# Optimization experiments

Hardware: AMD Instinct MI355X
Metric: run time of the kernel (lower is better)

The kernel has to match this reference:

```python
import jax, jax.numpy as jnp
import numpy as np

D = 1024   # cfg.hid (downscaled from 8192)
M = 20000  # cfg.mem_c // 2 (downscaled)
B, LQ = 4, 8
PLAST_S = 0.05
IMPORTANCE = 1.0


def mha_shared_kv(q, kv_k, kv_v, Wi, bi, Wo, bo, nheads):
    """torch nn.MultiheadAttention (batch_first) with batch-shared K/V.
    q: [B,Lq,D]; kv_k/kv_v: [Lk,D] shared across batch (avoids the .repeat()
    materialization in the original torch code while computing identical math)."""
    dh = D // nheads
    Wq, Wk, Wv = jnp.split(Wi, 3, axis=0)
    bq, bk, bv = jnp.split(bi, 3)
    qp = (jnp.einsum('bqd,ed->bqe', q, Wq) + bq) * (dh ** -0.5)
    kp = kv_k @ Wk.T + bk              # [Lk,D]
    vp = kv_v @ Wv.T + bv              # [Lk,D]
    qh = qp.reshape(q.shape[0], q.shape[1], nheads, dh)      # [B,Lq,h,dh]
    kh = kp.reshape(kp.shape[0], nheads, dh)                 # [Lk,h,dh]
    vh = vp.reshape(vp.shape[0], nheads, dh)                 # [Lk,h,dh]
    scores = jnp.einsum('bqhd,khd->bhqk', qh, kh)            # [B,h,Lq,Lk]
    attn = jax.nn.softmax(scores, axis=-1)
    ctx = jnp.einsum('bhqk,khd->bqhd', attn, vh)
    ctx = ctx.reshape(q.shape[0], q.shape[1], D)
    return ctx @ Wo.T + bo


def setup_inputs() -> dict:
    key = jax.random.key(0)
    ks = jax.random.split(key, 16)
    s = 0.02
    return {
        'q':    jax.random.normal(ks[0], (B, LQ, D), jnp.float32),
        'data': jax.random.normal(ks[1], (B, D), jnp.float32),
        'ek':   jax.random.normal(ks[2], (M, D), jnp.float32),
        'ev':   jax.random.normal(ks[3], (M, D), jnp.float32),
        'sk':   jax.random.normal(ks[4], (M, D), jnp.float32),
        'sv':   jax.random.normal(ks[5], (M, D), jnp.float32),
        'wm':   jax.random.normal(ks[6], (10, D), jnp.float32),
        'Wi_e': jax.random.normal(ks[7], (3 * D, D), jnp.float32) * s,
        'bi_e': jnp.zeros((3 * D,), jnp.float32),
        'Wo_e': jax.random.normal(ks[8], (D, D), jnp.float32) * s,
        'bo_e': jnp.zeros((D,), jnp.float32),
        'Wi_s': jax.random.normal(ks[9], (3 * D, D), jnp.float32) * s,
        'bi_s': jnp.zeros((3 * D,), jnp.float32),
        'Wo_s': jax.random.normal(ks[10], (D, D), jnp.float32) * s,
        'bo_s': jnp.zeros((D,), jnp.float32),
        'Wi_w': jax.random.normal(ks[11], (3 * D, D), jnp.float32) * s,
        'bi_w': jnp.zeros((3 * D,), jnp.float32),
        'Wo_w': jax.random.normal(ks[12], (D, D), jnp.float32) * s,
        'bo_w': jnp.zeros((D,), jnp.float32),
        'Wrp':  jax.random.normal(ks[13], (D, 3 * D), jnp.float32) * s,
        'brp':  jnp.zeros((D,), jnp.float32),
        'eu':   jnp.zeros((M,), jnp.float32),
    }


def reference(q, data, ek, ev, sk, sv, wm,
              Wi_e, bi_e, Wo_e, bo_e,
              Wi_s, bi_s, Wo_s, bo_s,
              Wi_w, bi_w, Wo_w, bo_w,
              Wrp, brp, eu):
    # ---- NeuroMemory.read ----
    e_r = mha_shared_kv(q, ek, ev, Wi_e, bi_e, Wo_e, bo_e, 16)
    s_r = mha_shared_kv(q, sk, sv, Wi_s, bi_s, Wo_s, bo_s, 16)
    w_r = mha_shared_kv(q, wm, wm, Wi_w, bi_w, Wo_w, bo_w, 8)
    read_out = jnp.concatenate([e_r, s_r, w_r], axis=-1) @ Wrp.T + brp  # [B,Lq,D]

    # ---- NeuroMemory.write (episodic, Hebbian plasticity update) ----
    scores = data @ ek.T                       # [B,M]
    probs = jax.nn.softmax(scores, axis=-1)    # [B,M]
    upd = probs * (PLAST_S * IMPORTANCE)       # [B,M]
    u = upd.mean(axis=0)[:, None]              # [M,1] (batch-mean update strength)
    d = data.mean(axis=0)[None, :]             # [1,D]
    new_ek = ek * (1.0 - u) + d * u            # [M,D]
    new_ev = ev * (1.0 - u) + d * u            # [M,D]
    new_eu = eu * 0.99 + jax.lax.stop_gradient(probs.sum(axis=0))  # [M]
    return (read_out, new_ek, new_ev, new_eu)
```

## Files before the change

### kernel.cpp

```cpp
#include <hip/hip_runtime.h>
#include <hip/hip_fp16.h>
#include <hip/hip_bf16.h>
#include <cstdint>
#include <cstddef>

#define D_HID 1024
#define MEM_M 20000
#define NBATCH 4
#define BL 32
#define NROWS 512
#define SROWS_E 516
#define SROWS_S 512
#define BK 32
#define LDT 40
#define PV_NC 16

typedef __attribute__((ext_vector_type(8))) short short8;
typedef __attribute__((ext_vector_type(4))) float f32x4;
typedef __attribute__((ext_vector_type(16))) float f32x16;
typedef __attribute__((ext_vector_type(4))) unsigned short us4;

__device__ inline ushort f2bf(float f) {
    __hip_bfloat16 b = __float2bfloat16(f);
    return *reinterpret_cast<ushort*>(&b);
}
__device__ inline float h2f(ushort u) {
    __half h; *reinterpret_cast<ushort*>(&h) = u; return __half2float(h);
}

__device__ __forceinline__ void block_sync_lds() {
    asm volatile("s_waitcnt lgkmcnt(0)" ::: "memory");
    __builtin_amdgcn_s_barrier();
}

struct SkDesc  { const float* A; const float* B; int K; int M; };
struct SkDescs { SkDesc d[5]; };
struct RdDesc  { const float* bias; float* dst; int M; int ldc; float alpha; };
struct RdDescs { RdDesc d[5]; };

__device__ __forceinline__ void skinny_body(const SkDesc dd, float* __restrict__ part,
                                            int gk, int k0, int n0, int tid)
{
    __shared__ float As[32][132];
    __shared__ float Bs[64][129];
    const int K = dd.K, M = dd.M;
    {
        const int r = tid >> 3, cbl = (tid & 7) * 16;
        if (r < M) {
            const float* src = dd.A + (size_t)r * K + k0 + cbl;
            #pragma unroll
            for (int i = 0; i < 4; ++i) {
                const float4 v = *(const float4*)(src + i * 4);
                As[r][cbl + i * 4 + 0] = v.x; As[r][cbl + i * 4 + 1] = v.y;
                As[r][cbl + i * 4 + 2] = v.z; As[r][cbl + i * 4 + 3] = v.w;
            }
        } else {
            #pragma unroll
            for (int i = 0; i < 16; ++i) As[r][cbl + i] = 0.f;
        }
    }
    {
        const int r = tid >> 2, cbl = (tid & 3) * 32;
        const float* src = dd.B + (size_t)(n0 + r) * K + k0 + cbl;
        #pragma unroll
        for (int i = 0; i < 8; ++i) {
            const float4 v = *(const float4*)(src + i * 4);
            Bs[r][cbl + i * 4 + 0] = v.x; Bs[r][cbl + i * 4 + 1] = v.y;
            Bs[r][cbl + i * 4 + 2] = v.z; Bs[r][cbl + i * 4 + 3] = v.w;
        }
    }
    __syncthreads();
    const int n = tid & 63, mg = tid >> 6;
    float acc[8];
    #pragma unroll
    for (int i = 0; i < 8; ++i) acc[i] = 0.f;
    #pragma unroll 4
    for (int k = 0; k < 128; k += 4) {
        const float b0 = Bs[n][k + 0], b1 = Bs[n][k + 1];
        const float b2 = Bs[n][k + 2], b3 = Bs[n][k + 3];
        #pragma unroll
        for (int i = 0; i < 8; ++i) {
            const float4 a = *(const float4*)&As[mg * 8 + i][k];
            acc[i] = fmaf(a.x, b0, fmaf(a.y, b1, fmaf(a.z, b2, fmaf(a.w, b3, acc[i]))));
        }
    }
    #pragma unroll
    for (int i = 0; i < 8; ++i)
        part[((size_t)gk * 32 + mg * 8 + i) * 1024 + n0 + n] = acc[i];
}

__global__ __launch_bounds__(256)
void k_skinny(SkDescs ds, float* __restrict__ part)
{
    skinny_body(ds.d[blockIdx.z], part,
                blockIdx.z * gridDim.y + blockIdx.y,
                blockIdx.y * 128, blockIdx.x * 64, threadIdx.x);
}

__global__ __launch_bounds__(256)
void k_head(SkDescs ds, float* __restrict__ part,
            const float* __restrict__ ek, const float* __restrict__ sk,
            ushort* __restrict__ kvb)
{
    const int bx = blockIdx.x;
    const int tid = threadIdx.x;
    if (bx < 640) {
        const int g = bx >> 7;
        const int rem = bx & 127;
        const int kc = rem >> 4;
        const int n0 = (rem & 15) * 64;
        skinny_body(ds.d[g], part, g * 8 + kc, kc * 128, n0, tid);
    } else {
        const size_t nchunks = (size_t)2 * MEM_M * D_HID / 8;
        for (size_t i = (size_t)(bx - 640) * 256 + tid; i < nchunks;
             i += (size_t)1408 * 256) {
            const size_t base = i * 8;
            const float* src = (base < (size_t)MEM_M * D_HID)
                             ? (ek + base) : (sk + base - (size_t)MEM_M * D_HID);
            const float4 v0 = *(const float4*)(src);
            const float4 v1 = *(const float4*)(src + 4);
            alignas(16) ushort o[8];
            o[0] = f2bf(v0.x); o[1] = f2bf(v0.y); o[2] = f2bf(v0.z); o[3] = f2bf(v0.w);
            o[4] = f2bf(v1.x); o[5] = f2bf(v1.y); o[6] = f2bf(v1.z); o[7] = f2bf(v1.w);
            *(short8*)(kvb + base) = *(const short8*)o;
        }
    }
}

__global__ __launch_bounds__(256)
void k_skred(RdDescs ds, const float* __restrict__ part, int nkc)
{
    const int g = blockIdx.y;
    const int m = blockIdx.x;
    const RdDesc dd = ds.d[g];
    if (m >= dd.M) return;
    const int c = threadIdx.x * 4;
    float4 s = make_float4(0.f, 0.f, 0.f, 0.f);
    for (int kc = 0; kc < nkc; ++kc) {
        const float4 v = *(const float4*)&part[((size_t)(g * nkc + kc) * 32 + m) * 1024 + c];
        s.x += v.x; s.y += v.y; s.z += v.z; s.w += v.w;
    }
    const float4 b = *(const float4*)(dd.bias + c);
    float4 o;
    o.x = (s.x + b.x) * dd.alpha; o.y = (s.y + b.y) * dd.alpha;
    o.z = (s.z + b.z) * dd.alpha; o.w = (s.w + b.w) * dd.alpha;
    *(float4*)(dd.dst + (size_t)m * dd.ldc + c) = o;
}

__global__ __launch_bounds__(256)
void mfma_scores(const ushort* __restrict__ A_e, const ushort* __restrict__ ekb,
                 const ushort* __restrict__ A_s, const ushort* __restrict__ skb,
                 __half* __restrict__ S_e, __half* __restrict__ S_s,
                 const float* __restrict__ c0_e, const float* __restrict__ c0_s)
{
    __shared__ ushort As[2][128][LDT];
    __shared__ ushort Bs[2][128][LDT];
    const int tid = threadIdx.x;
    const int i = blockIdx.x + 9 * blockIdx.y;
    const int xcd = i & 7, idx = i >> 3;
    const int wg = (xcd < 5 ? xcd * 177 : 885 + (xcd - 5) * 176) + idx;
    const int mi = wg % 9, nbk = wg / 9;
    const int bank = (mi >= 5);
    const int m0 = (bank ? (mi - 5) : mi) * 128;
    const int n0 = nbk * 128;
    const ushort* __restrict__ A = bank ? A_s : A_e;
    const ushort* __restrict__ B = bank ? skb : ekb;
    __half* __restrict__ S = bank ? S_s : S_e;
    const float* __restrict__ c0 = bank ? c0_s : c0_e;
    const int Mreal = bank ? SROWS_S : SROWS_E;

    const int wid = tid >> 6, lane = tid & 63;
    const int wr = (wid >> 1) * 64, wc = (wid & 1) * 64;
    const int l31 = lane & 31, l2 = lane >> 5;

    const int srow = tid >> 1;
    const int ac = (tid & 1) * 16;
    int gbrow = n0 + srow; if (gbrow > MEM_M - 1) gbrow = MEM_M - 1;
    const ushort* Ap = A + (size_t)(m0 + srow) * 1024 + ac;
    const ushort* Bp = B + (size_t)gbrow * 1024 + ac;

    f32x16 acc[2][2];
    #pragma unroll
    for (int fm = 0; fm < 2; ++fm)
        #pragma unroll
        for (int fn = 0; fn < 2; ++fn)
            #pragma unroll
            for (int r = 0; r < 16; ++r) acc[fm][fn][r] = 0.f;

    auto MF = [&](int bu) {
        short8 a[2][2], b[2][2];
        #pragma unroll
        for (int f = 0; f < 2; ++f)
            #pragma unroll
            for (int kh = 0; kh < 2; ++kh) {
                a[f][kh] = *(const short8*)&As[bu][wr + f * 32 + l31][kh * 16 + l2 * 8];
                b[f][kh] = *(const short8*)&Bs[bu][wc + f * 32 + l31][kh * 16 + l2 * 8];
            }
        #pragma unroll
        for (int fm = 0; fm < 2; ++fm)
            #pragma unroll
            for (int fn = 0; fn < 2; ++fn)
                #pragma unroll
                for (int kh = 0; kh < 2; ++kh)
                    acc[fm][fn] = __builtin_amdgcn_mfma_f32_32x32x16_bf16(
                        a[fm][kh], b[fn][kh], acc[fm][fn], 0, 0, 0);
    };

    short8 a00, a01, b00, b01;
    short8 a10, a11, b10, b11;

#define SC_LOAD0(KT) { a00 = *(const short8*)(Ap + (KT)); a01 = *(const short8*)(Ap + (KT) + 8); \
                       b00 = *(const short8*)(Bp + (KT)); b01 = *(const short8*)(Bp + (KT) + 8); }
#define SC_LOAD1(KT) { a10 = *(const short8*)(Ap + (KT)); a11 = *(const short8*)(Ap + (KT) + 8); \
                       b10 = *(const short8*)(Bp + (KT)); b11 = *(const short8*)(Bp + (KT) + 8); }
#define SC_STORE0(BU) { *(short8*)&As[BU][srow][ac] = a00; *(short8*)&As[BU][srow][ac + 8] = a01; \
                        *(short8*)&Bs[BU][srow][ac] = b00; *(short8*)&Bs[BU][srow][ac + 8] = b01; }
#define SC_STORE1(BU) { *(short8*)&As[BU][srow][ac] = a10; *(short8*)&As[BU][srow][ac + 8] = a11; \
                        *(short8*)&Bs[BU][srow][ac] = b10; *(short8*)&Bs[BU][srow][ac + 8] = b11; }

    SC_LOAD0(0);
    SC_LOAD1(32);
    SC_STORE0(0);
    block_sync_lds();
    for (int it = 0; it < 16; ++it) {
        const int kt = it * 64;
        if (it < 15) SC_LOAD0(kt + 64);
        MF(0);
        SC_STORE1(1);
        block_sync_lds();
        if (it < 15) SC_LOAD1(kt + 96);
        MF(1);
        if (it < 15) SC_STORE0(0);
        block_sync_lds();
    }
#undef SC_LOAD0
#undef SC_LOAD1
#undef SC_STORE0
#undef SC_STORE1

    #pragma unroll
    for (int fm = 0; fm < 2; ++fm) {
        #pragma unroll
        for (int fn = 0; fn < 2; ++fn) {
            #pragma unroll
            for (int r = 0; r < 16; ++r) {
                const int row = m0 + wr + fm * 32 + (r & 3) + 8 * (r >> 2) + 4 * l2;
                if (row >= Mreal) continue;
                const int col = n0 + wc + fn * 32 + l31;
                if (col < MEM_M)
                    S[(size_t)row * MEM_M + col] = __float2half(acc[fm][fn][r] + c0[row]);
            }
        }
    }
}

__global__ __launch_bounds__(256)
void mfma_pv(const ushort* __restrict__ P_e, const ushort* __restrict__ P_s,
             const float* __restrict__ ev, const float* __restrict__ sv,
             float* __restrict__ part)
{
    __shared__ ushort As[2][128][LDT];
    __shared__ ushort Bs[2][128][LDT];
    const int tid = threadIdx.x;
    const int z = blockIdx.z;
    const int bank = z >> 4, c = z & 15;
    const ushort* __restrict__ P = bank ? P_s : P_e;
    const float* __restrict__ V = bank ? sv : ev;
    const int m0 = blockIdx.y * 128, n0 = blockIdx.x * 128;
    const int ks0 = (c * 625) / PV_NC, ks1 = ((c + 1) * 625) / PV_NC;
    const int wid = tid >> 6, lane = tid & 63;
    const int wr = (wid >> 1) * 64, wc = (wid & 1) * 64;
    const int l31 = lane & 31, l2 = lane >> 5;
    const int kb = (tid & 7) * 4, nb2 = (tid >> 3) * 4;
    const int srow = tid >> 1, ac = (tid & 1) * 16;
    const ushort* Pp = P + (size_t)(m0 + srow) * MEM_M + ac;

    f32x16 acc[2][2];
    #pragma unroll
    for (int fm = 0; fm < 2; ++fm)
        #pragma unroll
        for (int fn = 0; fn < 2; ++fn)
            #pragma unroll
            for (int r = 0; r < 16; ++r) acc[fm][fn][r] = 0.f;

    auto MF = [&](int bu) {
        short8 a[2][2], b[2][2];
        #pragma unroll
        for (int f = 0; f < 2; ++f)
            #pragma unroll
            for (int kh = 0; kh < 2; ++kh) {
                a[f][kh] = *(const short8*)&As[bu][wr + f * 32 + l31][kh * 16 + l2 * 8];
                b[f][kh] = *(const short8*)&Bs[bu][wc + f * 32 + l31][kh * 16 + l2 * 8];
            }
        #pragma unroll
        for (int fm = 0; fm < 2; ++fm)
            #pragma unroll
            for (int fn = 0; fn < 2; ++fn)
                #pragma unroll
                for (int kh = 0; kh < 2; ++kh)
                    acc[fm][fn] = __builtin_amdgcn_mfma_f32_32x32x16_bf16(
                        a[fm][kh], b[fn][kh], acc[fm][fn], 0, 0, 0);
    };

    short8 pa00, pa01, pa10, pa11;
    float4 q00, q01, q02, q03, q10, q11, q12, q13;

#define PV_LOAD0(T) { const int kt = (T) * 32; \
    pa00 = *(const short8*)(Pp + kt); pa01 = *(const short8*)(Pp + kt + 8); \
    q00 = *(const float4*)(V + (size_t)(kt + kb + 0) * 1024 + n0 + nb2); \
    q01 = *(const float4*)(V + (size_t)(kt + kb + 1) * 1024 + n0 + nb2); \
    q02 = *(const float4*)(V + (size_t)(kt + kb + 2) * 1024 + n0 + nb2); \
    q03 = *(const float4*)(V + (size_t)(kt + kb + 3) * 1024 + n0 + nb2); }
#define PV_LOAD1(T) { const int kt = (T) * 32; \
    pa10 = *(const short8*)(Pp + kt); pa11 = *(const short8*)(Pp + kt + 8); \
    q10 = *(const float4*)(V + (size_t)(kt + kb + 0) * 1024 + n0 + nb2); \
    q11 = *(const float4*)(V + (size_t)(kt + kb + 1) * 1024 + n0 + nb2); \
    q12 = *(const float4*)(V + (size_t)(kt + kb + 2) * 1024 + n0 + nb2); \
    q13 = *(const float4*)(V + (size_t)(kt + kb + 3) * 1024 + n0 + nb2); }
#define PV_STORE0(BU) { \
    *(short8*)&As[BU][srow][ac] = pa00; *(short8*)&As[BU][srow][ac + 8] = pa01; \
    us4 w; \
    w.x = f2bf(q00.x); w.y = f2bf(q01.x); w.z = f2bf(q02.x); w.w = f2bf(q03.x); \
    *(us4*)&Bs[BU][nb2 + 0][kb] = w; \
    w.x = f2bf(q00.y); w.y = f2bf(q01.y); w.z = f2bf(q02.y); w.w = f2bf(q03.y); \
    *(us4*)&Bs[BU][nb2 + 1][kb] = w; \
    w.x = f2bf(q00.z); w.y = f2bf(q01.z); w.z = f2bf(q02.z); w.w = f2bf(q03.z); \
    *(us4*)&Bs[BU][nb2 + 2][kb] = w; \
    w.x = f2bf(q00.w); w.y = f2bf(q01.w); w.z = f2bf(q02.w); w.w = f2bf(q03.w); \
    *(us4*)&Bs[BU][nb2 + 3][kb] = w; }
#define PV_STORE1(BU) { \
    *(short8*)&As[BU][srow][ac] = pa10; *(short8*)&As[BU][srow][ac + 8] = pa11; \
    us4 w; \
    w.x = f2bf(q10.x); w.y = f2bf(q11.x); w.z = f2bf(q12.x); w.w = f2bf(q13.x); \
    *(us4*)&Bs[BU][nb2 + 0][kb] = w; \
    w.x = f2bf(q10.y); w.y = f2bf(q11.y); w.z = f2bf(q12.y); w.w = f2bf(q13.y); \
    *(us4*)&Bs[BU][nb2 + 1][kb] = w; \
    w.x = f2bf(q10.z); w.y = f2bf(q11.z); w.z = f2bf(q12.z); w.w = f2bf(q13.z); \
    *(us4*)&Bs[BU][nb2 + 2][kb] = w; \
    w.x = f2bf(q10.w); w.y = f2bf(q11.w); w.z = f2bf(q12.w); w.w = f2bf(q13.w); \
    *(us4*)&Bs[BU][nb2 + 3][kb] = w; }

    PV_LOAD0(ks0);
    if (ks0 + 1 < ks1) PV_LOAD1(ks0 + 1);
    PV_STORE0(0);
    block_sync_lds();
    for (int t = ks0; t < ks1; t += 2) {
        if (t + 2 < ks1) PV_LOAD0(t + 2);
        MF(0);
        if (t + 1 < ks1) PV_STORE1(1);
        block_sync_lds();
        if (t + 1 < ks1) {
            if (t + 3 < ks1) PV_LOAD1(t + 3);
            MF(1);
            if (t + 2 < ks1) PV_STORE0(0);
            block_sync_lds();
        }
    }
#undef PV_LOAD0
#undef PV_LOAD1
#undef PV_STORE0
#undef PV_STORE1

    float* __restrict__ po = part + (size_t)z * NROWS * 1024;
    #pragma unroll
    for (int fm = 0; fm < 2; ++fm)
        #pragma unroll
        for (int fn = 0; fn < 2; ++fn)
            #pragma unroll
            for (int r = 0; r < 16; ++r) {
                const int row = m0 + wr + fm * 32 + (r & 3) + 8 * (r >> 2) + 4 * l2;
                const int col = n0 + wc + fn * 32 + l31;
                po[(size_t)row * 1024 + col] = acc[fm][fn][r];
            }
}

__global__ __launch_bounds__(256)
void k_T(const float* __restrict__ qp,
         const float* __restrict__ Wi_e, const float* __restrict__ bi_e,
         const float* __restrict__ Wi_s, const float* __restrict__ bi_s,
         ushort* __restrict__ A_e, float* __restrict__ c0_e,
         ushort* __restrict__ A_s, float* __restrict__ c0_s,
         const float* __restrict__ data, float* __restrict__ dmean)
{
    const int bq = blockIdx.x;
    const int tid = threadIdx.x;
    if (bq >= 128) {
        if (bq < 252) {
            const int row = SROWS_E + (bq - 128);
            us4 z4; z4.x = 0; z4.y = 0; z4.z = 0; z4.w = 0;
            *(us4*)(A_e + (size_t)row * 1024 + tid * 4) = z4;
        } else {
            for (int t = tid; t < D_HID; t += 256) {
                float s = 0.f;
                #pragma unroll
                for (int b = 0; b < NBATCH; ++b) s += data[b * D_HID + t];
                dmean[t] = 0.25f * s;
                #pragma unroll
                for (int b = 0; b < NBATCH; ++b)
                    A_e[(size_t)(NROWS + b) * 1024 + t] = f2bf(data[b * D_HID + t]);
            }
            if (tid < NBATCH) c0_e[NROWS + tid] = 0.f;
        }
        return;
    }
    const int bank = bq >> 6;
    const int h = (bq >> 2) & 15;
    const int q4 = bq & 3;
    const float* qpB = qp + (size_t)bank * BL * D_HID;
    const float* Wk = (bank ? Wi_s : Wi_e) + (size_t)D_HID * D_HID;
    const float* bk = (bank ? bi_s : bi_e) + D_HID;
    ushort* T  = bank ? A_s : A_e;
    float* c0 = bank ? c0_s : c0_e;

    __shared__ float qs[32][64];
    for (int i = tid; i < 32 * 64; i += 256) {
        const int r = i >> 6, j = i & 63;
        qs[r][j] = qpB[(size_t)r * D_HID + h * 64 + j];
    }
    __syncthreads();
    const int e = q4 * 256 + tid;
    float acc[32];
    #pragma unroll
    for (int r = 0; r < 32; ++r) acc[r] = 0.f;
    for (int j = 0; j < 64; ++j) {
        const float w = Wk[(size_t)(h * 64 + j) * D_HID + e];
        #pragma unroll
        for (int r = 0; r < 32; ++r) acc[r] = fmaf(qs[r][j], w, acc[r]);
    }
    #pragma unroll
    for (int r = 0; r < 32; ++r) T[(size_t)(r * 16 + h) * 1024 + e] = f2bf(acc[r]);
    if (q4 == 0 && tid < 32) {
        float s = 0.f;
        for (int j = 0; j < 64; ++j) s += qs[tid][j] * bk[h * 64 + j];
        c0[tid * 16 + h] = s;
    }
}

__global__ __launch_bounds__(256)
void k_softmax(__half* __restrict__ S_e, __half* __restrict__ S_s,
               float* __restrict__ mrow, float* __restrict__ lrow)
{
    const int row = blockIdx.x;
    ushort* p = (row < SROWS_E) ? (ushort*)(S_e + (size_t)row * MEM_M)
                                : (ushort*)(S_s + (size_t)(row - SROWS_E) * MEM_M);
    const bool conv = (row < SROWS_E) ? (row < NROWS) : true;
    __shared__ float red_m[256];
    __shared__ float red_l[256];
    const int tid = threadIdx.x;
    float m = -3.0e38f, l = 0.f;
    for (int c = tid; c < MEM_M / 8; c += 256) {
        alignas(16) ushort t[8];
        *(short8*)t = *(const short8*)(p + c * 8);
        float v[8];
        #pragma unroll
        for (int j = 0; j < 8; ++j) v[j] = h2f(t[j]);
        float cm = v[0];
        #pragma unroll
        for (int j = 1; j < 8; ++j) cm = fmaxf(cm, v[j]);
        const float nm = fmaxf(m, cm);
        float s = 0.f;
        #pragma unroll
        for (int j = 0; j < 8; ++j) s += __expf(v[j] - nm);
        l = l * __expf(m - nm) + s;
        m = nm;
    }
    red_m[tid] = m; red_l[tid] = l; __syncthreads();
    for (int s = 128; s > 0; s >>= 1) {
        if (tid < s) {
            const float m2 = fmaxf(red_m[tid], red_m[tid + s]);
            red_l[tid] = red_l[tid] * __expf(red_m[tid] - m2)
                       + red_l[tid + s] * __expf(red_m[tid + s] - m2);
            red_m[tid] = m2;
        }
        __syncthreads();
    }
    const float rm = red_m[0];
    if (conv) {
        for (int c = tid; c < MEM_M / 8; c += 256) {
            alignas(16) ushort t[8];
            *(short8*)t = *(const short8*)(p + c * 8);
            alignas(16) ushort o[8];
            #pragma unroll
            for (int j = 0; j < 8; ++j) o[j] = f2bf(__expf(h2f(t[j]) - rm));
            *(short8*)(p + c * 8) = *(const short8*)o;
        }
    }
    if (tid == 0) { mrow[row] = rm; lrow[row] = red_l[0]; }
}

__global__ __launch_bounds__(256)
void k_uk(const __half* __restrict__ S_e,
          const float* __restrict__ mrow, const float* __restrict__ lrow,
          const float* __restrict__ eu,
          float* __restrict__ u, float* __restrict__ out_eu)
{
    const int k = blockIdx.x * 256 + threadIdx.x;
    if (k >= MEM_M) return;
    float sp = 0.f;
    #pragma unroll
    for (int b = 0; b < NBATCH; ++b) {
        const int row = NROWS + b;
        sp += __expf(__half2float(S_e[(size_t)row * MEM_M + k]) - mrow[row]) / lrow[row];
    }
    u[k] = 0.05f * 0.25f * sp;
    out_eu[k] = eu[k] * 0.99f + sp;
}

__global__ __launch_bounds__(256)
void k_pvred_upd(const float* __restrict__ part, const float* __restrict__ lrow,
                 float* __restrict__ R,
                 const float* __restrict__ ev, const float* __restrict__ u,
                 const float* __restrict__ dmean, float* __restrict__ out_ev)
{
    const int tid = threadIdx.x;
    if (blockIdx.x < 1024) {
        const size_t perb4 = (size_t)NROWS * 1024 / 4;
        const size_t i = (size_t)blockIdx.x * 256 + tid;
        const int bank = i >= perb4;
        const size_t off4 = i - (size_t)bank * perb4;
        const int m = (int)(off4 >> 8);
        const float inv = 1.f / lrow[bank ? (SROWS_E + m) : m];
        const float4* p = (const float4*)part + (size_t)bank * PV_NC * perb4 + off4;
        float4 s = make_float4(0.f, 0.f, 0.f, 0.f);
        #pragma unroll
        for (int c = 0; c < PV_NC; ++c) {
            const float4 v = p[(size_t)c * perb4];
            s.x += v.x; s.y += v.y; s.z += v.z; s.w += v.w;
        }
        s.x *= inv; s.y *= inv; s.z *= inv; s.w *= inv;
        ((float4*)R)[i] = s;
    } else {
        const int bid = blockIdx.x - 1024;
        const size_t n4 = (size_t)MEM_M * D_HID / 4;
        for (size_t i = (size_t)bid * 256 + tid; i < n4; i += (size_t)1024 * 256) {
            const int k = (int)(i >> 8);
            const int c = (int)(i & 255);
            const float uk = u[k];
            const float om = 1.f - uk;
            const float4 dd = ((const float4*)dmean)[c];
            const float4 b = ((const float4*)ev)[i];
            float4 ob;
            ob.x = b.x * om + dd.x * uk; ob.y = b.y * om + dd.y * uk;
            ob.z = b.z * om + dd.z * uk; ob.w = b.w * om + dd.w * uk;
            ((float4*)out_ev)[i] = ob;
        }
    }
}

__global__ __launch_bounds__(256)
void k_tail(const float* __restrict__ R,
            const float* __restrict__ Wi_e, const float* __restrict__ bi_e,
            const float* __restrict__ Wi_s, const float* __restrict__ bi_s,
            float* __restrict__ ctx,
            const float* __restrict__ qp, const float* __restrict__ kpw,
            const float* __restrict__ vpw,
            const float* __restrict__ ek, const float* __restrict__ u,
            const float* __restrict__ dmean, float* __restrict__ out_ek)
{
    __shared__ float sm[12384];
    const int tid = threadIdx.x;
    const int bx = blockIdx.x;
    if (bx < 32) {
        const int bank = bx >> 4;
        const int h = bx & 15;
        const float* Rb = R + (size_t)bank * NROWS * D_HID;
        const float* Wv = (bank ? Wi_s : Wi_e) + (size_t)2 * D_HID * D_HID;
        const float* bv = (bank ? bi_s : bi_e) + 2 * D_HID;
        float* cb = ctx + (size_t)bank * BL * D_HID;
        float (*Rs)[129] = (float(*)[129])sm;
        float (*Ws)[129] = (float(*)[129])(sm + 32 * 129);
        const int j = tid & 63;
        const int g = tid >> 6;
        float acc[8];
        #pragma unroll
        for (int i = 0; i < 8; ++i) acc[i] = 0.f;
        for (int ec = 0; ec < D_HID; ec += 128) {
            for (int i = tid; i < 32 * 128; i += 256) {
                const int r = i >> 7, e = i & 127;
                Rs[r][e] = Rb[(size_t)(r * 16 + h) * D_HID + ec + e];
            }
            for (int i = tid; i < 64 * 128; i += 256) {
                const int r = i >> 7, e = i & 127;
                Ws[r][e] = Wv[(size_t)(h * 64 + r) * D_HID + ec + e];
            }
            __syncthreads();
            for (int e = 0; e < 128; ++e) {
                const float w = Ws[j][e];
                #pragma unroll
                for (int i = 0; i < 8; ++i)
                    acc[i] = fmaf(Rs[g + 4 * i][e], w, acc[i]);
            }
            __syncthreads();
        }
        #pragma unroll
        for (int i = 0; i < 8; ++i) {
            const int bl = g + 4 * i;
            cb[(size_t)bl * D_HID + h * 64 + j] = acc[i] + bv[h * 64 + j];
        }
    } else if (bx < 64) {
        const int bl = bx - 32;
        float* q = sm;
        float (*kp)[1024] = (float(*)[1024])(sm + 1024);
        float (*pp)[10] = (float(*)[10])(sm + 1024 + 10240);
        const float* qrow = qp + (size_t)(2 * BL + bl) * D_HID;
        for (int i = tid; i < D_HID; i += 256) q[i] = qrow[i];
        for (int i = tid; i < 10 * D_HID; i += 256) kp[i >> 10][i & 1023] = kpw[i];
        __syncthreads();
        if (tid < 80) {
            const int h = tid / 10, k = tid % 10;
            float s = 0.f;
            for (int jj = 0; jj < 128; ++jj) s += q[h * 128 + jj] * kp[k][h * 128 + jj];
            pp[h][k] = s;
        }
        __syncthreads();
        if (tid < 8) {
            float m = -3.0e38f;
            for (int k = 0; k < 10; ++k) m = fmaxf(m, pp[tid][k]);
            float e[10]; float l = 0.f;
            for (int k = 0; k < 10; ++k) { e[k] = __expf(pp[tid][k] - m); l += e[k]; }
            const float inv = 1.f / l;
            for (int k = 0; k < 10; ++k) pp[tid][k] = e[k] * inv;
        }
        __syncthreads();
        float* cw = ctx + (size_t)(2 * BL + bl) * D_HID;
        for (int f = tid; f < D_HID; f += 256) {
            const int h = f >> 7;
            float s = 0.f;
            #pragma unroll
            for (int k = 0; k < 10; ++k) s += pp[h][k] * vpw[(size_t)k * D_HID + f];
            cw[f] = s;
        }
    } else {
        const int bid = bx - 64;
        const size_t n4 = (size_t)MEM_M * D_HID / 4;
        for (size_t i = (size_t)bid * 256 + tid; i < n4; i += (size_t)1024 * 256) {
            const int k = (int)(i >> 8);
            const int c = (int)(i & 255);
            const float uk = u[k];
            const float om = 1.f - uk;
            const float4 dd = ((const float4*)dmean)[c];
            const float4 a = ((const float4*)ek)[i];
            float4 oa;
            oa.x = a.x * om + dd.x * uk; oa.y = a.y * om + dd.y * uk;
            oa.z = a.z * om + dd.z * uk; oa.w = a.w * om + dd.w * uk;
            ((float4*)out_ek)[i] = oa;
        }
    }
}

extern "C" void kernel_launch(void* const* d_in, const int* in_sizes, int n_in,
                              void* d_out, int out_size, void* d_ws, size_t ws_size,
                              hipStream_t stream)
{
    (void)in_sizes; (void)n_in; (void)out_size; (void)ws_size;
    const float* q    = (const float*)d_in[0];
    const float* data = (const float*)d_in[1];
    const float* ek   = (const float*)d_in[2];
    const float* ev   = (const float*)d_in[3];
    const float* sk   = (const float*)d_in[4];
    const float* sv   = (const float*)d_in[5];
    const float* wm   = (const float*)d_in[6];
    const float* Wi_e = (const float*)d_in[7];
    const float* bi_e = (const float*)d_in[8];
    const float* Wo_e = (const float*)d_in[9];
    const float* bo_e = (const float*)d_in[10];
    const float* Wi_s = (const float*)d_in[11];
    const float* bi_s = (const float*)d_in[12];
    const float* Wo_s = (const float*)d_in[13];
    const float* bo_s = (const float*)d_in[14];
    const float* Wi_w = (const float*)d_in[15];
    const float* bi_w = (const float*)d_in[16];
    const float* Wo_w = (const float*)d_in[17];
    const float* bo_w = (const float*)d_in[18];
    const float* Wrp  = (const float*)d_in[19];
    const float* brp  = (const float*)d_in[20];
    const float* eu   = (const float*)d_in[21];

    float* out = (float*)d_out;
    float* out_read = out;
    float* out_ek = out + 32768;
    float* out_ev = out_ek + 20480000;
    float* out_eu = out_ev + 20480000;

    float* ws    = (float*)d_ws;
    float* qp    = ws;
    float* A_e   = qp + 98304;
    float* A_s   = A_e + 655360;
    float* c0_e  = A_s + 524288;
    float* c0_s  = c0_e + 640;
    float* dmean = c0_s + 512;
    float* u     = dmean + 1024;
    float* mrow  = u + 20480;
    float* lrow  = mrow + 1032;
    float* kpw   = lrow + 1032;
    float* vpw   = kpw + 10240;
    float* ctx   = vpw + 10240;
    float* cat   = ctx + 98304;
    float* skpart = cat + 98304;
    float* Rbuf  = skpart;

    ushort* A_e16 = (ushort*)A_e;
    ushort* A_s16 = (ushort*)A_s;

    ushort* ekb = (ushort*)out_ek;
    ushort* skb = ekb + (size_t)MEM_M * D_HID;
    float* part = out_ek;
    __half* S_e = (__half*)out_ev;
    __half* S_s = S_e + (size_t)SROWS_E * MEM_M;

    const dim3 b256(256);
    const float sc16 = 0.125f;
    const float sc8  = 0.08838834764831845f;

    SkDescs s1;
    s1.d[0] = {q,  Wi_e,            1024, 32};
    s1.d[1] = {q,  Wi_s,            1024, 32};
    s1.d[2] = {q,  Wi_w,            1024, 32};
    s1.d[3] = {wm, Wi_w + 1048576,  1024, 10};
    s1.d[4] = {wm, Wi_w + 2097152,  1024, 10};
    k_head<<<2048, b256, 0, stream>>>(s1, skpart, ek, sk, ekb);
    RdDescs r1;
    r1.d[0] = {bi_e,        qp,         32, 1024, sc16};
    r1.d[1] = {bi_s,        qp + 32768, 32, 1024, sc16};
    r1.d[2] = {bi_w,        qp + 65536, 32, 1024, sc8};
    r1.d[3] = {bi_w + 1024, kpw,        10, 1024, 1.f};
    r1.d[4] = {bi_w + 2048, vpw,        10, 1024, 1.f};
    k_skred<<<dim3(32, 5), b256, 0, stream>>>(r1, skpart, 8);

    k_T<<<253, b256, 0, stream>>>(qp, Wi_e, bi_e, Wi_s, bi_s,
                                  A_e16, c0_e, A_s16, c0_s, data, dmean);

    mfma_scores<<<dim3(9, 157), b256, 0, stream>>>(A_e16, ekb, A_s16, skb,
                                                   S_e, S_s, c0_e, c0_s);

    k_softmax<<<SROWS_E + SROWS_S, b256, 0, stream>>>(S_e, S_s, mrow, lrow);
    k_uk<<<79, b256, 0, stream>>>(S_e, mrow, lrow, eu, u, out_eu);

    mfma_pv<<<dim3(8, 4, 2 * PV_NC), b256, 0, stream>>>(
        (const ushort*)S_e, (const ushort*)S_s, ev, sv, part);

    k_pvred_upd<<<2048, b256, 0, stream>>>(part, lrow, Rbuf, ev, u, dmean, out_ev);

    k_tail<<<1088, b256, 0, stream>>>(Rbuf, Wi_e, bi_e, Wi_s, bi_s, ctx,
                                      qp, kpw, vpw, ek, u, dmean, out_ek);

    SkDescs s2;
    s2.d[0] = {ctx,         Wo_e, 1024, 32};
    s2.d[1] = {ctx + 32768, Wo_s, 1024, 32};
    s2.d[2] = {ctx + 65536, Wo_w, 1024, 32};
    s2.d[3] = {ctx,         Wo_e, 1024, 32};
    s2.d[4] = {ctx,         Wo_e, 1024, 32};
    k_skinny<<<dim3(16, 8, 3), b256, 0, stream>>>(s2, skpart);
    RdDescs r2;
    r2.d[0] = {bo_e, cat,        32, 3072, 1.f};
    r2.d[1] = {bo_s, cat + 1024, 32, 3072, 1.f};
    r2.d[2] = {bo_w, cat + 2048, 32, 3072, 1.f};
    r2.d[3] = r2.d[0];
    r2.d[4] = r2.d[0];
    k_skred<<<dim3(32, 3), b256, 0, stream>>>(r2, skpart, 8);

    SkDescs s3;
    s3.d[0] = {cat, Wrp, 3072, 32};
    s3.d[1] = s3.d[0]; s3.d[2] = s3.d[0]; s3.d[3] = s3.d[0]; s3.d[4] = s3.d[0];
    k_skinny<<<dim3(16, 24, 1), b256, 0, stream>>>(s3, skpart);
    RdDescs r3;
    r3.d[0] = {brp, out_read, 32, 1024, 1.f};
    r3.d[1] = r3.d[0]; r3.d[2] = r3.d[0]; r3.d[3] = r3.d[0]; r3.d[4] = r3.d[0];
    k_skred<<<dim3(32, 1), b256, 0, stream>>>(r3, skpart, 24);
}
```

Before: 487.6 us.

## Pre-convert value banks to bf16 during softmax and remap PV workgroups

Extra blocks in the softmax launch convert ev and sv from fp32 to bf16 buffers, so the PV GEMM reads half the bytes and skips per-tile conversion. The PV kernel now uses fewer K-splits (8 instead of 16) and an XCD-aware swizzle of workgroup ids. The write-scores rows move to a separate scratch buffer so the output buffers can be repacked to hold the bf16 copies and partials. The cost is an extra pass of roughly 160 MB of fp32 reads and 80 MB of bf16 writes, and the PV grid is halved, which may reduce parallelism.

```diff
diff --git a/kernel.cpp b/kernel.cpp
--- a/kernel.cpp
+++ b/kernel.cpp
@@ -13,7 +13,7 @@
 #define SROWS_S 512
 #define BK 32
 #define LDT 40
-#define PV_NC 16
+#define PV_NC 8
 
 typedef __attribute__((ext_vector_type(8))) short short8;
 typedef __attribute__((ext_vector_type(4))) float f32x4;
@@ -151,6 +151,7 @@
 void mfma_scores(const ushort* __restrict__ A_e, const ushort* __restrict__ ekb,
                  const ushort* __restrict__ A_s, const ushort* __restrict__ skb,
                  __half* __restrict__ S_e, __half* __restrict__ S_s,
+                 __half* __restrict__ swr,
                  const float* __restrict__ c0_e, const float* __restrict__ c0_s)
 {
     __shared__ ushort As[2][128][LDT];
@@ -165,7 +166,6 @@
     const int n0 = nbk * 128;
     const ushort* __restrict__ A = bank ? A_s : A_e;
     const ushort* __restrict__ B = bank ? skb : ekb;
-    __half* __restrict__ S = bank ? S_s : S_e;
     const float* __restrict__ c0 = bank ? c0_s : c0_e;
     const int Mreal = bank ? SROWS_S : SROWS_E;
 
@@ -247,8 +247,11 @@
                 const int row = m0 + wr + fm * 32 + (r & 3) + 8 * (r >> 2) + 4 * l2;
                 if (row >= Mreal) continue;
                 const int col = n0 + wc + fn * 32 + l31;
-                if (col < MEM_M)
-                    S[(size_t)row * MEM_M + col] = __float2half(acc[fm][fn][r] + c0[row]);
+                if (col >= MEM_M) continue;
+                const __half hv = __float2half(acc[fm][fn][r] + c0[row]);
+                if (bank) S_s[(size_t)row * MEM_M + col] = hv;
+                else if (row < NROWS) S_e[(size_t)row * MEM_M + col] = hv;
+                else swr[(size_t)(row - NROWS) * MEM_M + col] = hv;
             }
         }
     }
@@ -256,17 +259,20 @@
 
 __global__ __launch_bounds__(256)
 void mfma_pv(const ushort* __restrict__ P_e, const ushort* __restrict__ P_s,
-             const float* __restrict__ ev, const float* __restrict__ sv,
+             const ushort* __restrict__ evb, const ushort* __restrict__ svb,
              float* __restrict__ part)
 {
     __shared__ ushort As[2][128][LDT];
     __shared__ ushort Bs[2][128][LDT];
     const int tid = threadIdx.x;
-    const int z = blockIdx.z;
-    const int bank = z >> 4, c = z & 15;
+    const int bid = blockIdx.x + 8 * (blockIdx.y + 4 * blockIdx.z);
+    const int wgs = (bid & 7) * 64 + (bid >> 3);
+    const int nI = wgs & 7, mI = (wgs >> 3) & 3;
+    const int z = wgs >> 5;
+    const int bank = z >> 3, c = z & 7;
     const ushort* __restrict__ P = bank ? P_s : P_e;
-    const float* __restrict__ V = bank ? sv : ev;
-    const int m0 = blockIdx.y * 128, n0 = blockIdx.x * 128;
+    const ushort* __restrict__ Vb = bank ? svb : evb;
+    const int m0 = mI * 128, n0 = nI * 128;
     const int ks0 = (c * 625) / PV_NC, ks1 = ((c + 1) * 625) / PV_NC;
     const int wid = tid >> 6, lane = tid & 63;
     const int wr = (wid >> 1) * 64, wc = (wid & 1) * 64;
@@ -303,41 +309,41 @@
     };
 
     short8 pa00, pa01, pa10, pa11;
-    float4 q00, q01, q02, q03, q10, q11, q12, q13;
+    us4 q0[4], q1[4];
 
 #define PV_LOAD0(T) { const int kt = (T) * 32; \
     pa00 = *(const short8*)(Pp + kt); pa01 = *(const short8*)(Pp + kt + 8); \
-    q00 = *(const float4*)(V + (size_t)(kt + kb + 0) * 1024 + n0 + nb2); \
-    q01 = *(const float4*)(V + (size_t)(kt + kb + 1) * 1024 + n0 + nb2); \
-    q02 = *(const float4*)(V + (size_t)(kt + kb + 2) * 1024 + n0 + nb2); \
-    q03 = *(const float4*)(V + (size_t)(kt + kb + 3) * 1024 + n0 + nb2); }
+    q0[0] = *(const us4*)(Vb + (size_t)(kt + kb + 0) * 1024 + n0 + nb2); \
+    q0[1] = *(const us4*)(Vb + (size_t)(kt + kb + 1) * 1024 + n0 + nb2); \
+    q0[2] = *(const us4*)(Vb + (size_t)(kt + kb + 2) * 1024 + n0 + nb2); \
+    q0[3] = *(const us4*)(Vb + (size_t)(kt + kb + 3) * 1024 + n0 + nb2); }
 #define PV_LOAD1(T) { const int kt = (T) * 32; \
     pa10 = *(const short8*)(Pp + kt); pa11 = *(const short8*)(Pp + kt + 8); \
-    q10 = *(const float4*)(V + (size_t)(kt + kb + 0) * 1024 + n0 + nb2); \
-    q11 = *(const float4*)(V + (size_t)(kt + kb + 1) * 1024 + n0 + nb2); \
-    q12 = *(const float4*)(V + (size_t)(kt + kb + 2) * 1024 + n0 + nb2); \
-    q13 = *(const float4*)(V + (size_t)(kt + kb + 3) * 1024 + n0 + nb2); }
+    q1[0] = *(const us4*)(Vb + (size_t)(kt + kb + 0) * 1024 + n0 + nb2); \
+    q1[1] = *(const us4*)(Vb + (size_t)(kt + kb + 1) * 1024 + n0 + nb2); \
+    q1[2] = *(const us4*)(Vb + (size_t)(kt + kb + 2) * 1024 + n0 + nb2); \
+    q1[3] = *(const us4*)(Vb + (size_t)(kt + kb + 3) * 1024 + n0 + nb2); }
 #define PV_STORE0(BU) { \
     *(short8*)&As[BU][srow][ac] = pa00; *(short8*)&As[BU][srow][ac + 8] = pa01; \
     us4 w; \
-    w.x = f2bf(q00.x); w.y = f2bf(q01.x); w.z = f2bf(q02.x); w.w = f2bf(q03.x); \
+    w.x = q0[0].x; w.y = q0[1].x; w.z = q0[2].x; w.w = q0[3].x; \
     *(us4*)&Bs[BU][nb2 + 0][kb] = w; \
-    w.x = f2bf(q00.y); w.y = f2bf(q01.y); w.z = f2bf(q02.y); w.w = f2bf(q03.y); \
+    w.x = q0[0].y; w.y = q0[1].y; w.z = q0[2].y; w.w = q0[3].y; \
     *(us4*)&Bs[BU][nb2 + 1][kb] = w; \
-    w.x = f2bf(q00.z); w.y = f2bf(q01.z); w.z = f2bf(q02.z); w.w = f2bf(q03.z); \
+    w.x = q0[0].z; w.y = q0[1].z; w.z = q0[2].z; w.w = q0[3].z; \
     *(us4*)&Bs[BU][nb2 + 2][kb] = w; \
-    w.x = f2bf(q00.w); w.y = f2bf(q01.w); w.z = f2bf(q02.w); w.w = f2bf(q03.w); \
+    w.x = q0[0].w; w.y = q0[1].w; w.z = q0[2].w; w.w = q0[3].w; \
     *(us4*)&Bs[BU][nb2 + 3][kb] = w; }
 #define PV_STORE1(BU) { \
     *(short8*)&As[BU][srow][ac] = pa10; *(short8*)&As[BU][srow][ac + 8] = pa11; \
     us4 w; \
-    w.x = f2bf(q10.x); w.y = f2bf(q11.x); w.z = f2bf(q12.x); w.w = f2bf(q13.x); \
+    w.x = q1[0].x; w.y = q1[1].x; w.z = q1[2].x; w.w = q1[3].x; \
     *(us4*)&Bs[BU][nb2 + 0][kb] = w; \
-    w.x = f2bf(q10.y); w.y = f2bf(q11.y); w.z = f2bf(q12.y); w.w = f2bf(q13.y); \
+    w.x = q1[0].y; w.y = q1[1].y; w.z = q1[2].y; w.w = q1[3].y; \
     *(us4*)&Bs[BU][nb2 + 1][kb] = w; \
-    w.x = f2bf(q10.z); w.y = f2bf(q11.z); w.z = f2bf(q12.z); w.w = f2bf(q13.z); \
+    w.x = q1[0].z; w.y = q1[1].z; w.z = q1[2].z; w.w = q1[3].z; \
     *(us4*)&Bs[BU][nb2 + 2][kb] = w; \
-    w.x = f2bf(q10.w); w.y = f2bf(q11.w); w.z = f2bf(q12.w); w.w = f2bf(q13.w); \
+    w.x = q1[0].w; w.y = q1[1].w; w.z = q1[2].w; w.w = q1[3].w; \
     *(us4*)&Bs[BU][nb2 + 3][kb] = w; }
 
     PV_LOAD0(ks0);
@@ -438,15 +444,37 @@
 
 __global__ __launch_bounds__(256)
 void k_softmax(__half* __restrict__ S_e, __half* __restrict__ S_s,
-               float* __restrict__ mrow, float* __restrict__ lrow)
-{
-    const int row = blockIdx.x;
-    ushort* p = (row < SROWS_E) ? (ushort*)(S_e + (size_t)row * MEM_M)
-                                : (ushort*)(S_s + (size_t)(row - SROWS_E) * MEM_M);
-    const bool conv = (row < SROWS_E) ? (row < NROWS) : true;
+               __half* __restrict__ swr,
+               float* __restrict__ mrow, float* __restrict__ lrow,
+               const float* __restrict__ ev, const float* __restrict__ sv,
+               ushort* __restrict__ evb, ushort* __restrict__ svb)
+{
+    const int bx = blockIdx.x;
+    const int tid = threadIdx.x;
+    if (bx >= SROWS_E + SROWS_S) {
+        const size_t nchunks = (size_t)2 * MEM_M * D_HID / 8;
+        for (size_t i = (size_t)(bx - (SROWS_E + SROWS_S)) * 256 + tid; i < nchunks;
+             i += (size_t)1408 * 256) {
+            const size_t base = i * 8;
+            const bool second = base >= (size_t)MEM_M * D_HID;
+            const float* src = second ? (sv + base - (size_t)MEM_M * D_HID) : (ev + base);
+            ushort* dst = second ? (svb + base - (size_t)MEM_M * D_HID) : (evb + base);
+            const float4 v0 = *(const float4*)(src);
+            const float4 v1 = *(const float4*)(src + 4);
+            alignas(16) ushort o[8];
+            o[0] = f2bf(v0.x); o[1] = f2bf(v0.y); o[2] = f2bf(v0.z); o[3] = f2bf(v0.w);
+            o[4] = f2bf(v1.x); o[5] = f2bf(v1.y); o[6] = f2bf(v1.z); o[7] = f2bf(v1.w);
+            *(short8*)dst = *(const short8*)o;
+        }
+        return;
+    }
+    const int row = bx;
+    ushort* p; bool conv = true;
+    if (row < NROWS) p = (ushort*)(S_e + (size_t)row * MEM_M);
+    else if (row < SROWS_E) { p = (ushort*)(swr + (size_t)(row - NROWS) * MEM_M); conv = false; }
+    else p = (ushort*)(S_s + (size_t)(row - SROWS_E) * MEM_M);
     __shared__ float red_m[256];
     __shared__ float red_l[256];
-    const int tid = threadIdx.x;
     float m = -3.0e38f, l = 0.f;
     for (int c = tid; c < MEM_M / 8; c += 256) {
         alignas(16) ushort t[8];
@@ -489,7 +517,7 @@
 }
 
 __global__ __launch_bounds__(256)
-void k_uk(const __half* __restrict__ S_e,
+void k_uk(const __half* __restrict__ swr,
           const float* __restrict__ mrow, const float* __restrict__ lrow,
           const float* __restrict__ eu,
           float* __restrict__ u, float* __restrict__ out_eu)
@@ -500,7 +528,7 @@
     #pragma unroll
     for (int b = 0; b < NBATCH; ++b) {
         const int row = NROWS + b;
-        sp += __expf(__half2float(S_e[(size_t)row * MEM_M + k]) - mrow[row]) / lrow[row];
+        sp += __expf(__half2float(swr[(size_t)b * MEM_M + k]) - mrow[row]) / lrow[row];
     }
     u[k] = 0.05f * 0.25f * sp;
     out_eu[k] = eu[k] * 0.99f + sp;
@@ -698,15 +726,18 @@
     float* cat   = ctx + 98304;
     float* skpart = cat + 98304;
     float* Rbuf  = skpart;
+    __half* swr  = (__half*)(skpart + 1310720);
 
     ushort* A_e16 = (ushort*)A_e;
     ushort* A_s16 = (ushort*)A_s;
 
     ushort* ekb = (ushort*)out_ek;
     ushort* skb = ekb + (size_t)MEM_M * D_HID;
-    float* part = out_ek;
+    ushort* evb = (ushort*)out_ek;
+    float* part = out_ek + 10240000;
     __half* S_e = (__half*)out_ev;
-    __half* S_s = S_e + (size_t)SROWS_E * MEM_M;
+    __half* S_s = S_e + (size_t)NROWS * MEM_M;
+    ushort* svb = (ushort*)(S_s + (size_t)NROWS * MEM_M);
 
     const dim3 b256(256);
     const float sc16 = 0.125f;
@@ -731,13 +762,14 @@
                                   A_e16, c0_e, A_s16, c0_s, data, dmean);
 
     mfma_scores<<<dim3(9, 157), b256, 0, stream>>>(A_e16, ekb, A_s16, skb,
-                                                   S_e, S_s, c0_e, c0_s);
-
-    k_softmax<<<SROWS_E + SROWS_S, b256, 0, stream>>>(S_e, S_s, mrow, lrow);
-    k_uk<<<79, b256, 0, stream>>>(S_e, mrow, lrow, eu, u, out_eu);
+                                                   S_e, S_s, swr, c0_e, c0_s);
+
+    k_softmax<<<SROWS_E + SROWS_S + 1408, b256, 0, stream>>>(
+        S_e, S_s, swr, mrow, lrow, ev, sv, evb, svb);
+    k_uk<<<79, b256, 0, stream>>>(swr, mrow, lrow, eu, u, out_eu);
 
     mfma_pv<<<dim3(8, 4, 2 * PV_NC), b256, 0, stream>>>(
-        (const ushort*)S_e, (const ushort*)S_s, ev, sv, part);
+        (const ushort*)S_e, (const ushort*)S_s, evb, svb, part);
 
     k_pvred_upd<<<2048, b256, 0, stream>>>(part, lrow, Rbuf, ev, u, dmean, out_ev);
 
```

Result: slower. 497.8 us (+2.1%).
